# Optimization experiments

Hardware: AMD Instinct MI355X
Metric: run time of the kernel (lower is better)

The kernel has to match this reference:

```python
import jax, jax.numpy as jnp
import numpy as np
import math

CEN_W = 1.0
ANG_W = 1.0


def _radius(ndim):
    # Iterative version of the recursive Radius() from the source.
    if ndim < 1:
        raise ValueError('ndim >= 1 required')
    if ndim == 1:
        return 0.0
    r = 0.5
    for _ in range(3, ndim + 1):
        r = 0.5 / math.sqrt(1.0 - r * r)
    return r


def _costheta(ndim):
    return 2.0 * _radius(ndim - 1) ** 2 - 1.0


def setup_inputs() -> dict:
    key = jax.random.key(0)
    k1, k2, k3 = jax.random.split(key, 3)
    B, C, D = 65536, 1000, 512
    y = jax.random.randint(k1, (B,), 0, C, dtype=jnp.int64 if jax.config.jax_enable_x64 else jnp.int32)
    feat = jax.random.normal(k2, (B, D), dtype=jnp.float32)
    centers = jax.random.normal(k3, (C, D), dtype=jnp.float32)
    return {"y": y, "feat": feat, "centers": centers}


def reference(y, feat, centers):
    C = centers.shape[0]
    B = feat.shape[0]
    ct = jnp.float32(_costheta(C))  # static Python constant from num_classes

    # ---- center loss: gather assigned centers, squared diff sum ----
    centers_pred = centers[y]                      # [B, D] gather
    diff = feat - centers_pred
    loss_cen = 0.5 * jnp.sum(diff * diff) / B

    # ---- angular loss: vectorized Gram matrix over classes ----
    # In torch, centers[j].data and dist are detached -> stop_gradient here.
    centers_sg = jax.lax.stop_gradient(centers)
    dist = jnp.linalg.norm(centers_sg, axis=1)     # [C], detached
    gram = centers @ centers_sg.T                  # [C, C]; grad flows via rows only
    sim = gram / (dist[:, None] * dist[None, :])
    offdiag = 1.0 - jnp.eye(C, dtype=sim.dtype)
    loss_ang = jnp.sum(offdiag * (sim - ct) ** 2) / (0.5 * C * (C - 1))

    return loss_cen * CEN_W + loss_ang * ANG_W
```

## Files before the change

kernel.cpp:

```cpp
#include <hip/hip_runtime.h>
#include <math.h>

typedef __attribute__((ext_vector_type(8))) short bf16x8;
typedef __attribute__((ext_vector_type(4))) float f32x4;
typedef __attribute__((ext_vector_type(4))) float vf4;

__device__ __forceinline__ float wave_reduce(float v) {
#pragma unroll
    for (int off = 32; off > 0; off >>= 1) v += __shfl_down(v, off, 64);
    return v;
}

__device__ __forceinline__ unsigned short f2bf(float x) {
    unsigned u = __float_as_uint(x);
    u += 0x7FFFu + ((u >> 16) & 1u);
    return (unsigned short)(u >> 16);
}

__global__ __launch_bounds__(256) void one_kernel(const int* __restrict__ y,
                                                  const vf4* __restrict__ feat4,
                                                  const vf4* __restrict__ cent4,
                                                  float* __restrict__ out,
                                                  int n4, int d4, float cen_scale,
                                                  int C, int ntile, int steps,
                                                  float ct, float ang_scale,
                                                  int ang_blocks, int center_blocks) {
    const int bid = blockIdx.x;
    const int lane = threadIdx.x & 63;
    const int wid = threadIdx.x >> 6;
    __shared__ float sm[4];

    float partial = 0.f;

    if (bid < ang_blocks) {
        const int wglob = bid * 4 + wid;
        const int wstride = ang_blocks * 4;
        const int n = lane & 15;
        const int quad = lane >> 4;
        const int ntile2 = ntile * ntile;
        float local = 0.f;
        for (int t = wglob; t < ntile2; t += wstride) {
            const int ti = t / ntile;
            const int tj = t - ti * ntile;
            const int ra = ti * 16 + n;
            const int rb = tj * 16 + n;
            const bool va = ra < C;
            const bool vb = rb < C;
            const vf4* aptr = cent4 + (size_t)ra * d4 + quad * 2;
            const vf4* bptr = cent4 + (size_t)rb * d4 + quad * 2;
            f32x4 acc = {0.f, 0.f, 0.f, 0.f};
            float sa = 0.f, sb = 0.f;
#pragma unroll 4
            for (int st = 0; st < steps; ++st) {
                vf4 a0 = {0.f, 0.f, 0.f, 0.f}, a1 = a0, b0 = a0, b1 = a0;
                if (va) { a0 = aptr[st * 8]; a1 = aptr[st * 8 + 1]; }
                if (vb) { b0 = bptr[st * 8]; b1 = bptr[st * 8 + 1]; }
                sa += a0.x * a0.x + a0.y * a0.y + a0.z * a0.z + a0.w * a0.w
                    + a1.x * a1.x + a1.y * a1.y + a1.z * a1.z + a1.w * a1.w;
                sb += b0.x * b0.x + b0.y * b0.y + b0.z * b0.z + b0.w * b0.w
                    + b1.x * b1.x + b1.y * b1.y + b1.z * b1.z + b1.w * b1.w;
                bf16x8 af, bf;
                af[0] = (short)f2bf(a0.x); af[1] = (short)f2bf(a0.y);
                af[2] = (short)f2bf(a0.z); af[3] = (short)f2bf(a0.w);
                af[4] = (short)f2bf(a1.x); af[5] = (short)f2bf(a1.y);
                af[6] = (short)f2bf(a1.z); af[7] = (short)f2bf(a1.w);
                bf[0] = (short)f2bf(b0.x); bf[1] = (short)f2bf(b0.y);
                bf[2] = (short)f2bf(b0.z); bf[3] = (short)f2bf(b0.w);
                bf[4] = (short)f2bf(b1.x); bf[5] = (short)f2bf(b1.y);
                bf[6] = (short)f2bf(b1.z); bf[7] = (short)f2bf(b1.w);
                acc = __builtin_amdgcn_mfma_f32_16x16x32_bf16(af, bf, acc, 0, 0, 0);
            }
            sa += __shfl_xor(sa, 16, 64); sa += __shfl_xor(sa, 32, 64);
            sb += __shfl_xor(sb, 16, 64); sb += __shfl_xor(sb, 32, 64);
            float di[4];
#pragma unroll
            for (int rr = 0; rr < 4; ++rr) di[rr] = __shfl(sa, quad * 4 + rr, 64);
            const int gj = tj * 16 + n;
            const float dj = sb;
#pragma unroll
            for (int rr = 0; rr < 4; ++rr) {
                const int gi = ti * 16 + quad * 4 + rr;
                if (gi < C && gj < C && gi != gj) {
                    float sim = acc[rr] * rsqrtf(di[rr] * dj);
                    float dlt = sim - ct;
                    local += dlt * dlt;
                }
            }
        }
        partial = local * ang_scale;
    } else {
        const int cb = bid - ang_blocks;
        const int stride = center_blocks * 256;
        float s = 0.f;
        int i = cb * 256 + threadIdx.x;
        if ((stride % d4) == 0) {
            if (i < n4) {
                int row = i / d4;
                const int col = i - row * d4;
                const int rstep = stride / d4;
                for (; i < n4; i += stride, row += rstep) {
                    const int cls = y[row];
                    vf4 f = __builtin_nontemporal_load(feat4 + i);
                    vf4 c = cent4[(size_t)cls * d4 + col];
                    float dx = f.x - c.x, dy = f.y - c.y, dz = f.z - c.z, dw = f.w - c.w;
                    s += dx * dx + dy * dy + dz * dz + dw * dw;
                }
            }
        } else {
            for (; i < n4; i += stride) {
                int row = i / d4;
                int col = i - row * d4;
                const int cls = y[row];
                vf4 f = __builtin_nontemporal_load(feat4 + i);
                vf4 c = cent4[(size_t)cls * d4 + col];
                float dx = f.x - c.x, dy = f.y - c.y, dz = f.z - c.z, dw = f.w - c.w;
                s += dx * dx + dy * dy + dz * dz + dw * dw;
            }
        }
        partial = s * cen_scale;
    }

    float r = wave_reduce(partial);
    if (lane == 0) sm[wid] = r;
    __syncthreads();
    if (threadIdx.x == 0) {
        atomicAdd(out, sm[0] + sm[1] + sm[2] + sm[3]);
    }
}

extern "C" void kernel_launch(void* const* d_in, const int* in_sizes, int n_in,
                              void* d_out, int out_size, void* d_ws, size_t ws_size,
                              hipStream_t stream) {
    const int* y = (const int*)d_in[0];
    const float* feat = (const float*)d_in[1];
    const float* centers = (const float*)d_in[2];

    const int B = in_sizes[0];
    const int D = in_sizes[1] / B;
    const int C = in_sizes[2] / D;
    const int d4 = D / 4;
    const int ntile = (C + 15) / 16;

    const int nd = C - 1;
    double r = 0.0;
    if (nd >= 2) {
        r = 0.5;
        for (int i = 3; i <= nd; ++i) r = 0.5 / sqrt(1.0 - r * r);
    }
    const float ct = (float)(2.0 * r * r - 1.0);

    const float cen_scale = (float)(0.5 / (double)B);
    const float ang_scale = (float)(1.0 / (0.5 * (double)C * (double)(C - 1)));

    const int ang_blocks = 256;
    const int center_blocks = 1792;

    one_kernel<<<ang_blocks + center_blocks, 256, 0, stream>>>(
        y, (const vf4*)feat, (const vf4*)centers, (float*)d_out,
        B * d4, d4, cen_scale, C, ntile, D / 32, ct, ang_scale,
        ang_blocks, center_blocks);
}
```

Measured before the change: 235.4 us.

## Spread Gram tiles across all blocks and use truncating bf16 packing

Replaces the fixed split between angular-loss blocks and center-loss blocks with a scheme where each wave computes at most one 16x16 Gram tile and then every block also streams its share of the center-loss data. This is meant to remove the load imbalance of a few blocks looping over many MFMA tiles. The bf16 conversion is also changed from round-to-nearest-even to truncation with packed dword assembly, cutting ALU work per step at a small cost in precision.

```diff
diff --git a/kernel.cpp b/kernel.cpp
--- a/kernel.cpp
+++ b/kernel.cpp
@@ -4,6 +4,7 @@
 typedef __attribute__((ext_vector_type(8))) short bf16x8;
 typedef __attribute__((ext_vector_type(4))) float f32x4;
 typedef __attribute__((ext_vector_type(4))) float vf4;
+typedef __attribute__((ext_vector_type(4))) unsigned int u32x4;
 
 __device__ __forceinline__ float wave_reduce(float v) {
 #pragma unroll
@@ -11,10 +12,9 @@
     return v;
 }
 
-__device__ __forceinline__ unsigned short f2bf(float x) {
-    unsigned u = __float_as_uint(x);
-    u += 0x7FFFu + ((u >> 16) & 1u);
-    return (unsigned short)(u >> 16);
+__device__ __forceinline__ unsigned int pk_trunc(float f0, float f1) {
+    unsigned u0 = __float_as_uint(f0), u1 = __float_as_uint(f1);
+    return (u1 & 0xFFFF0000u) | (u0 >> 16);
 }
 
 __global__ __launch_bounds__(256) void one_kernel(const int* __restrict__ y,
@@ -23,8 +23,7 @@
                                                   float* __restrict__ out,
                                                   int n4, int d4, float cen_scale,
                                                   int C, int ntile, int steps,
-                                                  float ct, float ang_scale,
-                                                  int ang_blocks, int center_blocks) {
+                                                  float ct, float ang_scale) {
     const int bid = blockIdx.x;
     const int lane = threadIdx.x & 63;
     const int wid = threadIdx.x >> 6;
@@ -32,67 +31,63 @@
 
     float partial = 0.f;
 
-    if (bid < ang_blocks) {
-        const int wglob = bid * 4 + wid;
-        const int wstride = ang_blocks * 4;
+    const int t = bid * 4 + wid;
+    const int ntile2 = ntile * ntile;
+    if (t < ntile2) {
+        const int ti = t / ntile;
+        const int tj = t - ti * ntile;
         const int n = lane & 15;
         const int quad = lane >> 4;
-        const int ntile2 = ntile * ntile;
+        const int ra = ti * 16 + n;
+        const int rb = tj * 16 + n;
+        const bool va = ra < C;
+        const bool vb = rb < C;
+        const vf4* aptr = cent4 + (size_t)ra * d4 + quad * 2;
+        const vf4* bptr = cent4 + (size_t)rb * d4 + quad * 2;
+        f32x4 acc = {0.f, 0.f, 0.f, 0.f};
+        float sa = 0.f, sb = 0.f;
+#pragma unroll 4
+        for (int st = 0; st < steps; ++st) {
+            vf4 a0 = {0.f, 0.f, 0.f, 0.f}, a1 = a0, b0 = a0, b1 = a0;
+            if (va) { a0 = aptr[st * 8]; a1 = aptr[st * 8 + 1]; }
+            if (vb) { b0 = bptr[st * 8]; b1 = bptr[st * 8 + 1]; }
+            sa += a0.x * a0.x + a0.y * a0.y + a0.z * a0.z + a0.w * a0.w
+                + a1.x * a1.x + a1.y * a1.y + a1.z * a1.z + a1.w * a1.w;
+            sb += b0.x * b0.x + b0.y * b0.y + b0.z * b0.z + b0.w * b0.w
+                + b1.x * b1.x + b1.y * b1.y + b1.z * b1.z + b1.w * b1.w;
+            u32x4 ap, bp;
+            ap.x = pk_trunc(a0.x, a0.y); ap.y = pk_trunc(a0.z, a0.w);
+            ap.z = pk_trunc(a1.x, a1.y); ap.w = pk_trunc(a1.z, a1.w);
+            bp.x = pk_trunc(b0.x, b0.y); bp.y = pk_trunc(b0.z, b0.w);
+            bp.z = pk_trunc(b1.x, b1.y); bp.w = pk_trunc(b1.z, b1.w);
+            bf16x8 af = __builtin_bit_cast(bf16x8, ap);
+            bf16x8 bf = __builtin_bit_cast(bf16x8, bp);
+            acc = __builtin_amdgcn_mfma_f32_16x16x32_bf16(af, bf, acc, 0, 0, 0);
+        }
+        sa += __shfl_xor(sa, 16, 64); sa += __shfl_xor(sa, 32, 64);
+        sb += __shfl_xor(sb, 16, 64); sb += __shfl_xor(sb, 32, 64);
+        float di[4];
+#pragma unroll
+        for (int rr = 0; rr < 4; ++rr) di[rr] = __shfl(sa, quad * 4 + rr, 64);
+        const int gj = tj * 16 + n;
+        const float dj = sb;
         float local = 0.f;
-        for (int t = wglob; t < ntile2; t += wstride) {
-            const int ti = t / ntile;
-            const int tj = t - ti * ntile;
-            const int ra = ti * 16 + n;
-            const int rb = tj * 16 + n;
-            const bool va = ra < C;
-            const bool vb = rb < C;
-            const vf4* aptr = cent4 + (size_t)ra * d4 + quad * 2;
-            const vf4* bptr = cent4 + (size_t)rb * d4 + quad * 2;
-            f32x4 acc = {0.f, 0.f, 0.f, 0.f};
-            float sa = 0.f, sb = 0.f;
-#pragma unroll 4
-            for (int st = 0; st < steps; ++st) {
-                vf4 a0 = {0.f, 0.f, 0.f, 0.f}, a1 = a0, b0 = a0, b1 = a0;
-                if (va) { a0 = aptr[st * 8]; a1 = aptr[st * 8 + 1]; }
-                if (vb) { b0 = bptr[st * 8]; b1 = bptr[st * 8 + 1]; }
-                sa += a0.x * a0.x + a0.y * a0.y + a0.z * a0.z + a0.w * a0.w
-                    + a1.x * a1.x + a1.y * a1.y + a1.z * a1.z + a1.w * a1.w;
-                sb += b0.x * b0.x + b0.y * b0.y + b0.z * b0.z + b0.w * b0.w
-                    + b1.x * b1.x + b1.y * b1.y + b1.z * b1.z + b1.w * b1.w;
-                bf16x8 af, bf;
-                af[0] = (short)f2bf(a0.x); af[1] = (short)f2bf(a0.y);
-                af[2] = (short)f2bf(a0.z); af[3] = (short)f2bf(a0.w);
-                af[4] = (short)f2bf(a1.x); af[5] = (short)f2bf(a1.y);
-                af[6] = (short)f2bf(a1.z); af[7] = (short)f2bf(a1.w);
-                bf[0] = (short)f2bf(b0.x); bf[1] = (short)f2bf(b0.y);
-                bf[2] = (short)f2bf(b0.z); bf[3] = (short)f2bf(b0.w);
-                bf[4] = (short)f2bf(b1.x); bf[5] = (short)f2bf(b1.y);
-                bf[6] = (short)f2bf(b1.z); bf[7] = (short)f2bf(b1.w);
-                acc = __builtin_amdgcn_mfma_f32_16x16x32_bf16(af, bf, acc, 0, 0, 0);
-            }
-            sa += __shfl_xor(sa, 16, 64); sa += __shfl_xor(sa, 32, 64);
-            sb += __shfl_xor(sb, 16, 64); sb += __shfl_xor(sb, 32, 64);
-            float di[4];
 #pragma unroll
-            for (int rr = 0; rr < 4; ++rr) di[rr] = __shfl(sa, quad * 4 + rr, 64);
-            const int gj = tj * 16 + n;
-            const float dj = sb;
-#pragma unroll
-            for (int rr = 0; rr < 4; ++rr) {
-                const int gi = ti * 16 + quad * 4 + rr;
-                if (gi < C && gj < C && gi != gj) {
-                    float sim = acc[rr] * rsqrtf(di[rr] * dj);
-                    float dlt = sim - ct;
-                    local += dlt * dlt;
-                }
+        for (int rr = 0; rr < 4; ++rr) {
+            const int gi = ti * 16 + quad * 4 + rr;
+            if (gi < C && gj < C && gi != gj) {
+                float sim = acc[rr] * rsqrtf(di[rr] * dj);
+                float dlt = sim - ct;
+                local += dlt * dlt;
             }
         }
         partial = local * ang_scale;
-    } else {
-        const int cb = bid - ang_blocks;
-        const int stride = center_blocks * 256;
+    }
+
+    {
+        const int stride = gridDim.x * 256;
         float s = 0.f;
-        int i = cb * 256 + threadIdx.x;
+        int i = bid * 256 + threadIdx.x;
         if ((stride % d4) == 0) {
             if (i < n4) {
                 int row = i / d4;
@@ -117,7 +112,7 @@
                 s += dx * dx + dy * dy + dz * dz + dw * dw;
             }
         }
-        partial = s * cen_scale;
+        partial += s * cen_scale;
     }
 
     float r = wave_reduce(partial);
@@ -152,11 +147,7 @@
     const float cen_scale = (float)(0.5 / (double)B);
     const float ang_scale = (float)(1.0 / (0.5 * (double)C * (double)(C - 1)));
 
-    const int ang_blocks = 256;
-    const int center_blocks = 1792;
-
-    one_kernel<<<ang_blocks + center_blocks, 256, 0, stream>>>(
+    one_kernel<<<2048, 256, 0, stream>>>(
         y, (const vf4*)feat, (const vf4*)centers, (float*)d_out,
-        B * d4, d4, cen_scale, C, ntile, D / 32, ct, ang_scale,
-        ang_blocks, center_blocks);
+        B * d4, d4, cen_scale, C, ntile, D / 32, ct, ang_scale);
 }
```

Result: faster. 222.0 us (-5.7%).
